# Performance work log

Hardware: AMD Instinct MI355X
Metric: run time of the kernel (lower is better)

Reference implementation:

```python
import jax, jax.numpy as jnp
import numpy as np

N = 100000   # num nodes
E = 1600000  # num edges (before self-loops)
D_IN, D_HID, D_OUT = 128, 128, 64


def _gcn_layer(x, W, b, src, dst, norm):
    # GCNConv: h = x @ W, then normalized sparse aggregation, then bias.
    h = x @ W                              # [N, d_out]
    msg = h[src] * norm[:, None]           # [E+N, d_out] gathered + scaled messages
    out = jax.ops.segment_sum(msg, dst, num_segments=N)  # scatter-add to dst nodes
    return out + b


def reference(x, W1, b1, W2, b2, edge_index):
    src0, dst0 = edge_index[0], edge_index[1]
    # GCNConv adds self-loops by default
    loop = jnp.arange(N, dtype=src0.dtype)
    src = jnp.concatenate([src0, loop])
    dst = jnp.concatenate([dst0, loop])
    # symmetric normalization: deg^{-1/2}[src] * deg^{-1/2}[dst]
    deg = jax.ops.segment_sum(jnp.ones_like(src, dtype=x.dtype), dst, num_segments=N)
    dinv = jnp.where(deg > 0, jax.lax.rsqrt(jnp.maximum(deg, 1.0)), 0.0)
    norm = dinv[src] * dinv[dst]           # [E+N]

    h = jax.nn.relu(_gcn_layer(x, W1, b1, src, dst, norm))
    return _gcn_layer(h, W2, b2, src, dst, norm)


def setup_inputs() -> dict:
    key = jax.random.key(0)
    k1, k2, k3, k4 = jax.random.split(key, 4)
    x = jax.random.normal(k1, (N, D_IN), dtype=jnp.float32)
    # glorot-ish init for weights
    W1 = jax.random.normal(k2, (D_IN, D_HID), dtype=jnp.float32) * (1.0 / np.sqrt(D_IN))
    b1 = jnp.zeros((D_HID,), dtype=jnp.float32)
    W2 = jax.random.normal(k3, (D_HID, D_OUT), dtype=jnp.float32) * (1.0 / np.sqrt(D_HID))
    b2 = jnp.zeros((D_OUT,), dtype=jnp.float32)
    edge_index = jax.random.randint(k4, (2, E), 0, N, dtype=jnp.int64)
    return {"x": x, "W1": W1, "b1": b1, "W2": W2, "b2": b2, "edge_index": edge_index}
```

## Files before the change

### kernel.cpp

```cpp
#include <hip/hip_runtime.h>

static constexpr int NN = 100000;
static constexpr int EE = 1600000;
static constexpr int BSZ = 64;
static constexpr int NB = (NN + BSZ - 1) / BSZ;
static constexpr int BCAP = 2048;
static constexpr int TILE = 2048;
static constexpr int GB = 2048;


__device__ __forceinline__ unsigned short f2bf(float f) {
    unsigned u = __float_as_uint(f);
    u += 0x7FFFu + ((u >> 16) & 1u);
    return (unsigned short)(u >> 16);
}
__device__ __forceinline__ float bfl(unsigned u) { return __uint_as_float(u << 16); }
__device__ __forceinline__ float bfh(unsigned u) { return __uint_as_float(u & 0xFFFF0000u); }

typedef __attribute__((ext_vector_type(8))) short short8;
typedef __attribute__((ext_vector_type(4))) float float4v;
typedef __attribute__((ext_vector_type(4))) float float4n;


__global__ __launch_bounds__(256) void k_init(const float* __restrict__ W1,
                                              const float* __restrict__ W2,
                                              unsigned short* __restrict__ W1t,
                                              unsigned short* __restrict__ W2t,
                                              int* __restrict__ bcur) {
    int idx = blockIdx.x * 256 + threadIdx.x;
    if (idx < 16384) {
        int n = idx >> 7, k = idx & 127;
        W1t[idx] = f2bf(W1[k * 128 + n]);
    } else if (idx < 24576) {
        int j = idx - 16384;
        int n = j >> 7, k = j & 127;
        W2t[j] = f2bf(W2[k * 64 + n]);
    } else if (idx < 24576 + NB) {
        int b = idx - 24576;
        bcur[b] = b * BCAP;
    }
}


__global__ __launch_bounds__(256) void k_bin(const int* __restrict__ src,
                                             const int* __restrict__ dst,
                                             int* __restrict__ bcur,
                                             int* __restrict__ ebuf, int E) {
    constexpr int K = TILE / 256;
    __shared__ int lcnt[NB];
    __shared__ int lbase[NB];
    const int t = threadIdx.x;
    const int e0 = blockIdx.x * TILE;

    for (int i = t; i < NB; i += 256) lcnt[i] = 0;
    __syncthreads();

    int dreg[K], ofs[K];
#pragma unroll
    for (int k = 0; k < K; ++k) {
        int e = e0 + k * 256 + t;
        if (e < E) {
            int d = dst[e];
            dreg[k] = d;
            ofs[k] = atomicAdd(&lcnt[d >> 6], 1);
        } else dreg[k] = -1;
    }
    __syncthreads();

    for (int i = t; i < NB; i += 256) {
        int c = lcnt[i];
        lbase[i] = c ? atomicAdd(&bcur[i], c) : 0;
    }
    __syncthreads();

#pragma unroll
    for (int k = 0; k < K; ++k) {
        if (dreg[k] >= 0) {
            int e = e0 + k * 256 + t;
            int s = src[e];
            int b = dreg[k] >> 6;
            ebuf[lbase[b] + ofs[k]] = (s << 6) | (dreg[k] & 63);
        }
    }
}


__global__ __launch_bounds__(256) void k_csr(const int* __restrict__ bcur,
                                             const int* __restrict__ ebuf,
                                             int2* __restrict__ rbe,
                                             float* __restrict__ dinv,
                                             int* __restrict__ csr, int n) {
    __shared__ int lcnt[BSZ];
    __shared__ int lofs[BSZ];
    const int b = blockIdx.x, t = threadIdx.x;
    if (t < BSZ) lcnt[t] = 0;
    __syncthreads();
    const int beg = b * BCAP, end = bcur[b];
    for (int j = beg + t; j < end; j += 256) atomicAdd(&lcnt[ebuf[j] & 63], 1);
    __syncthreads();
    if (t < BSZ) {
        int c = lcnt[t];
        int x = c;
#pragma unroll
        for (int off = 1; off < 64; off <<= 1) {
            int y = __shfl_up(x, off, 64);
            if (t >= off) x += y;
        }
        int exc = x - c;
        int node = b * BSZ + t;
        if (node < n) {
            rbe[node] = make_int2(beg + exc, beg + exc + c);
            dinv[node] = rsqrtf((float)c + 1.0f);
        }
        lofs[t] = beg + exc;
    }
    __syncthreads();
    for (int j = beg + t; j < end; j += 256) {
        int e = ebuf[j];
        int pos = atomicAdd(&lofs[e & 63], 1);
        csr[pos] = e >> 6;
    }
}


__global__ __launch_bounds__(256) void k_gemm128m(const float* __restrict__ X,
                                                  const unsigned short* __restrict__ W1t,
                                                  const float* __restrict__ dinv,
                                                  unsigned* __restrict__ G, int M) {
    __shared__ float cls[4 * 16 * 132];
    const int t = threadIdx.x;
    const int w = t >> 6, lane = t & 63;
    const int quad = lane >> 4, m16 = lane & 15;
    const int row0 = blockIdx.x * 64 + w * 16;
    int arow = row0 + m16; if (arow >= M) arow = M - 1;

    short8 afrag[4];
#pragma unroll
    for (int ks = 0; ks < 4; ++ks) {
        const float* p = X + (size_t)arow * 128 + ks * 32 + quad * 8;
        float4 u0 = ((const float4*)p)[0];
        float4 u1 = ((const float4*)p)[1];
        short8 a;
        a[0] = (short)f2bf(u0.x); a[1] = (short)f2bf(u0.y);
        a[2] = (short)f2bf(u0.z); a[3] = (short)f2bf(u0.w);
        a[4] = (short)f2bf(u1.x); a[5] = (short)f2bf(u1.y);
        a[6] = (short)f2bf(u1.z); a[7] = (short)f2bf(u1.w);
        afrag[ks] = a;
    }
    float* myc = cls + w * 16 * 132;
#pragma unroll
    for (int nt = 0; nt < 8; ++nt) {
        float4v acc = {0.f, 0.f, 0.f, 0.f};
#pragma unroll
        for (int ks = 0; ks < 4; ++ks) {
            const short8 b = *((const short8*)(W1t + (size_t)(nt * 16 + m16) * 128 + ks * 32 + quad * 8));
            acc = __builtin_amdgcn_mfma_f32_16x16x32_bf16(afrag[ks], b, acc, 0, 0, 0);
        }
#pragma unroll
        for (int r = 0; r < 4; ++r)
            myc[(quad * 4 + r) * 132 + nt * 16 + m16] = acc[r];
    }
    __syncthreads();
#pragma unroll
    for (int i = 0; i < 8; ++i) {
        int idx = i * 64 + lane;
        int r = idx >> 5, c = idx & 31;
        int grow = row0 + r;
        if (grow < M) {
            float4 v = *((const float4*)(myc + r * 132 + c * 4));
            float s = dinv[grow];
            uint2 p;
            p.x = (unsigned)f2bf(v.x * s) | ((unsigned)f2bf(v.y * s) << 16);
            p.y = (unsigned)f2bf(v.z * s) | ((unsigned)f2bf(v.w * s) << 16);
            ((uint2*)G)[(size_t)(c >> 3) * NN * 8 + (size_t)grow * 8 + (c & 7)] = p;
        }
    }
}


__global__ __launch_bounds__(256) void k_gemm64m(const unsigned short* __restrict__ X,
                                                 const unsigned short* __restrict__ W2t,
                                                 const float* __restrict__ dinv,
                                                 unsigned* __restrict__ G, int M) {
    __shared__ float cls[4 * 16 * 68];
    const int t = threadIdx.x;
    const int w = t >> 6, lane = t & 63;
    const int quad = lane >> 4, m16 = lane & 15;
    const int row0 = blockIdx.x * 64 + w * 16;
    int arow = row0 + m16; if (arow >= M) arow = M - 1;

    short8 afrag[4];
#pragma unroll
    for (int ks = 0; ks < 4; ++ks)
        afrag[ks] = *((const short8*)(X + (size_t)ks * NN * 32 + (size_t)arow * 32 + quad * 8));

    float* myc = cls + w * 16 * 68;
#pragma unroll
    for (int nt = 0; nt < 4; ++nt) {
        float4v acc = {0.f, 0.f, 0.f, 0.f};
#pragma unroll
        for (int ks = 0; ks < 4; ++ks) {
            const short8 b = *((const short8*)(W2t + (size_t)(nt * 16 + m16) * 128 + ks * 32 + quad * 8));
            acc = __builtin_amdgcn_mfma_f32_16x16x32_bf16(afrag[ks], b, acc, 0, 0, 0);
        }
#pragma unroll
        for (int r = 0; r < 4; ++r)
            myc[(quad * 4 + r) * 68 + nt * 16 + m16] = acc[r];
    }
    __syncthreads();
#pragma unroll
    for (int i = 0; i < 4; ++i) {
        int idx = i * 64 + lane;
        int r = idx >> 4, c = idx & 15;
        int grow = row0 + r;
        if (grow < M) {
            float4 v = *((const float4*)(myc + r * 68 + c * 4));
            float s = dinv[grow];
            uint2 p;
            p.x = (unsigned)f2bf(v.x * s) | ((unsigned)f2bf(v.y * s) << 16);
            p.y = (unsigned)f2bf(v.z * s) | ((unsigned)f2bf(v.w * s) << 16);
            ((uint2*)G)[(size_t)(c >> 3) * NN * 8 + (size_t)grow * 8 + (c & 7)] = p;
        }
    }
}


__device__ __forceinline__ int2 ld_rbe(const int2* __restrict__ rbe, int node, int n) {
    int2 r = make_int2(0, 0);
    if (node < n) {
        long long v = __builtin_nontemporal_load((const long long*)(rbe + node));
        r.x = (int)(v & 0xffffffffll);
        r.y = (int)(v >> 32);
    }
    return r;
}
__device__ __forceinline__ int ld_csr(const int* __restrict__ csr, int2 re, int off) {
    int deg = re.y - re.x;
    int v = __builtin_nontemporal_load(csr + re.x + ((off < deg) ? off : 0));
    return (deg > 0) ? v : 0;
}

template<int LAYER>
__global__ __launch_bounds__(256) void k_gather_s(
        const int2* __restrict__ rbe, const int* __restrict__ csr,
        const unsigned* __restrict__ Gall, const float* __restrict__ dinv,
        const float* __restrict__ bias, unsigned* __restrict__ OUT, int n) {
    const int lane = threadIdx.x & 63;
    const int w = threadIdx.x >> 6;
    const int l16 = lane & 15;
    const int g2 = (lane >> 3) & 1;
    const int sub = lane & 7;

    int slice, wis, stride;
    if (LAYER == 1) {
        slice = (blockIdx.x & 7) >> 1;
        wis = (blockIdx.x >> 3) * 8 + (blockIdx.x & 1) * 4 + w;
        stride = (GB / 8) * 8;
    } else {
        slice = (blockIdx.x & 7) >> 2;
        wis = (blockIdx.x >> 3) * 16 + (blockIdx.x & 3) * 4 + w;
        stride = (GB / 8) * 16;
    }
    const int iter_nodes = stride * 4;
    const uint2* slab = (const uint2*)(Gall + (size_t)slice * NN * 16);

    int node = wis * 4 + (lane >> 4);
    int2 re_cur = ld_rbe(rbe, node, n);
    int2 re_nx  = ld_rbe(rbe, node + iter_nodes, n);
    int idx_cur = ld_csr(csr, re_cur, l16);

    for (; node < n; node += iter_nodes) {
        const int2 re = re_cur;
        int idx = idx_cur;
        re_cur = re_nx;
        re_nx  = ld_rbe(rbe, node + 2 * iter_nodes, n);
        idx_cur = ld_csr(csr, re_cur, l16);

        const int deg = re.y - re.x;
        int idx2 = (deg > 16) ? ld_csr(csr, re, 16 + l16) : 0;

        float a0 = 0.f, a1 = 0.f, a2 = 0.f, a3 = 0.f;
        int wb = 0;
        bool done = false;
        while (!done) {
#pragma unroll
            for (int half = 0; half < 2 && !done; ++half) {
                const int hbase = wb + half * 16;
                const int hidx = half ? idx2 : idx;
#pragma unroll
                for (int g = 0; g < 2 && !done; ++g) {
#pragma unroll
                    for (int st = 0; st < 4; ++st) {
                        int ew = g * 8 + st * 2 + g2;
                        int e = hbase + ew;
                        int s = __shfl(hidx, (lane & 48) | ew, 64);
                        uint2 v = slab[(size_t)s * 8 + sub];
                        if (e < deg) { a0 += bfl(v.x); a1 += bfh(v.x);
                                       a2 += bfl(v.y); a3 += bfh(v.y); }
                    }
                    if (!__any(hbase + (g + 1) * 8 < deg)) done = true;
                }
            }
            if (!done) {
                wb += 32;
                if (wb >= BCAP) break;
                idx  = ld_csr(csr, re, wb + l16);
                idx2 = (deg > wb + 16) ? ld_csr(csr, re, wb + 16 + l16) : 0;
            }
        }
        a0 += __shfl_xor(a0, 8, 64);
        a1 += __shfl_xor(a1, 8, 64);
        a2 += __shfl_xor(a2, 8, 64);
        a3 += __shfl_xor(a3, 8, 64);
        if (g2 == 0) {
            uint2 vs = slab[(size_t)node * 8 + sub];
            a0 += bfl(vs.x); a1 += bfh(vs.x); a2 += bfl(vs.y); a3 += bfh(vs.y);
            const float di = dinv[node];
            const float4 bv = ((const float4*)bias)[slice * 8 + sub];
            float r0 = fmaf(a0, di, bv.x), r1 = fmaf(a1, di, bv.y);
            float r2 = fmaf(a2, di, bv.z), r3 = fmaf(a3, di, bv.w);
            if (LAYER == 1) {
                r0 = fmaxf(r0, 0.f); r1 = fmaxf(r1, 0.f);
                r2 = fmaxf(r2, 0.f); r3 = fmaxf(r3, 0.f);
                unsigned lo = (unsigned)f2bf(r0) | ((unsigned)f2bf(r1) << 16);
                unsigned hi = (unsigned)f2bf(r2) | ((unsigned)f2bf(r3) << 16);
                unsigned long long p = (unsigned long long)lo | ((unsigned long long)hi << 32);
                __builtin_nontemporal_store(p,
                    (unsigned long long*)((uint2*)OUT + (size_t)slice * NN * 8 + (size_t)node * 8 + sub));
            } else {
                float4n r = {r0, r1, r2, r3};
                __builtin_nontemporal_store(r,
                    (float4n*)OUT + (size_t)node * 16 + slice * 8 + sub);
            }
        }
    }
}


extern "C" void kernel_launch(void* const* d_in, const int* in_sizes, int n_in,
                              void* d_out, int out_size, void* d_ws, size_t ws_size,
                              hipStream_t stream) {
    const float* x  = (const float*)d_in[0];
    const float* W1 = (const float*)d_in[1];
    const float* b1 = (const float*)d_in[2];
    const float* W2 = (const float*)d_in[3];
    const float* b2 = (const float*)d_in[4];
    const int*   ei = (const int*)d_in[5];
    const int* src = ei;
    const int* dst = ei + EE;
    float* out = (float*)d_out;

    unsigned* g1b = (unsigned*)d_ws;
    unsigned* h1b = g1b + (size_t)NN * 64;
    unsigned* g2b = h1b + (size_t)NN * 64;
    unsigned short* w1t = (unsigned short*)(g2b + (size_t)NN * 32);
    unsigned short* w2t = w1t + 16384;
    int2*  rbe  = (int2*)(w2t + 8192);
    float* dinv = (float*)(rbe + NN);
    int*   bcur = (int*)(dinv + NN);
    int*   ebuf = bcur + NB;
    int*   csr  = ebuf + (size_t)NB * BCAP;

    constexpr int IB = (24576 + NB + 255) / 256;

    k_init<<<IB, 256, 0, stream>>>(W1, W2, w1t, w2t, bcur);
    k_bin<<<(EE + TILE - 1) / TILE, 256, 0, stream>>>(src, dst, bcur, ebuf, EE);
    k_csr<<<NB, 256, 0, stream>>>(bcur, ebuf, rbe, dinv, csr, NN);

    k_gemm128m<<<(NN + 63) / 64, 256, 0, stream>>>(x, w1t, dinv, g1b, NN);
    k_gather_s<1><<<GB, 256, 0, stream>>>(rbe, csr, g1b, dinv, b1, h1b, NN);

    k_gemm64m<<<(NN + 63) / 64, 256, 0, stream>>>((const unsigned short*)h1b, w2t, dinv, g2b, NN);
    k_gather_s<2><<<GB, 256, 0, stream>>>(rbe, csr, g2b, dinv, b2, (unsigned*)out, NN);
}
```

Before: 350.7 us.

## Split gather by source-node half to localize feature reads in cache

Each destination's CSR neighbor list is split into two segments by whether the source id is in the low or high half of the node range. The gather then runs as separate passes, one per source half, so each pass touches only half the feature table and its working set fits better in cache. Partial sums from the first pass are stored in fp32 scratch, reusing the g2b and ebuf workspace, and the second pass adds them in and applies scaling, bias and activation. The lane mapping also changes to 8 lanes per node. The price is more kernel launches and extra partial-sum traffic through global memory.

After: 402.3 us. 1.15x slower.

```diff
diff --git a/kernel.cpp b/kernel.cpp
--- a/kernel.cpp
+++ b/kernel.cpp
@@ -1,6 +1,8 @@
 #include <hip/hip_runtime.h>
 
 static constexpr int NN = 100000;
+static constexpr int NH = NN / 2;
+static constexpr int NNH2 = NN / 2;
 static constexpr int EE = 1600000;
 static constexpr int BSZ = 64;
 static constexpr int NB = (NN + BSZ - 1) / BSZ;
@@ -87,19 +89,24 @@
 
 __global__ __launch_bounds__(256) void k_csr(const int* __restrict__ bcur,
                                              const int* __restrict__ ebuf,
-                                             int2* __restrict__ rbe,
+                                             int2* __restrict__ seg0,
+                                             int2* __restrict__ seg1,
                                              float* __restrict__ dinv,
                                              int* __restrict__ csr, int n) {
-    __shared__ int lcnt[BSZ];
-    __shared__ int lofs[BSZ];
+    __shared__ int lcnt_lo[BSZ], lcnt_hi[BSZ];
+    __shared__ int lofs_lo[BSZ], lofs_hi[BSZ];
     const int b = blockIdx.x, t = threadIdx.x;
-    if (t < BSZ) lcnt[t] = 0;
+    if (t < BSZ) { lcnt_lo[t] = 0; lcnt_hi[t] = 0; }
     __syncthreads();
     const int beg = b * BCAP, end = bcur[b];
-    for (int j = beg + t; j < end; j += 256) atomicAdd(&lcnt[ebuf[j] & 63], 1);
+    for (int j = beg + t; j < end; j += 256) {
+        int e = ebuf[j];
+        if ((e >> 6) < NH) atomicAdd(&lcnt_lo[e & 63], 1);
+        else               atomicAdd(&lcnt_hi[e & 63], 1);
+    }
     __syncthreads();
     if (t < BSZ) {
-        int c = lcnt[t];
+        int lo = lcnt_lo[t], hi = lcnt_hi[t], c = lo + hi;
         int x = c;
 #pragma unroll
         for (int off = 1; off < 64; off <<= 1) {
@@ -109,16 +116,19 @@
         int exc = x - c;
         int node = b * BSZ + t;
         if (node < n) {
-            rbe[node] = make_int2(beg + exc, beg + exc + c);
+            seg0[node] = make_int2(beg + exc, beg + exc + lo);
+            seg1[node] = make_int2(beg + exc + lo, beg + exc + c);
             dinv[node] = rsqrtf((float)c + 1.0f);
         }
-        lofs[t] = beg + exc;
+        lofs_lo[t] = beg + exc;
+        lofs_hi[t] = beg + exc + lo;
     }
     __syncthreads();
     for (int j = beg + t; j < end; j += 256) {
         int e = ebuf[j];
-        int pos = atomicAdd(&lofs[e & 63], 1);
-        csr[pos] = e >> 6;
+        int d = e & 63, s = e >> 6;
+        int pos = atomicAdd((s < NH) ? &lofs_lo[d] : &lofs_hi[d], 1);
+        csr[pos] = s;
     }
 }
 
@@ -225,112 +235,131 @@
 }
 
 
-__device__ __forceinline__ int2 ld_rbe(const int2* __restrict__ rbe, int node, int n) {
+__device__ __forceinline__ int2 ld_seg(const int2* __restrict__ seg, int node, int nend) {
     int2 r = make_int2(0, 0);
-    if (node < n) {
-        long long v = __builtin_nontemporal_load((const long long*)(rbe + node));
+    if (node < nend) {
+        long long v = __builtin_nontemporal_load((const long long*)(seg + node));
         r.x = (int)(v & 0xffffffffll);
         r.y = (int)(v >> 32);
     }
     return r;
 }
-__device__ __forceinline__ int ld_csr(const int* __restrict__ csr, int2 re, int off) {
-    int deg = re.y - re.x;
-    int v = __builtin_nontemporal_load(csr + re.x + ((off < deg) ? off : 0));
-    return (deg > 0) ? v : 0;
-}
-
-template<int LAYER>
-__global__ __launch_bounds__(256) void k_gather_s(
-        const int2* __restrict__ rbe, const int* __restrict__ csr,
+__device__ __forceinline__ int ld_csr8(const int* __restrict__ csr, int b, int d, int off) {
+    int o = (off < d) ? off : (d > 0 ? d - 1 : 0);
+    return __builtin_nontemporal_load(csr + b + o);
+}
+
+template<int LAYER, int HALF>
+__global__ __launch_bounds__(256) void k_gather_h(
+        const int2* __restrict__ seg, const int* __restrict__ csr,
         const unsigned* __restrict__ Gall, const float* __restrict__ dinv,
-        const float* __restrict__ bias, unsigned* __restrict__ OUT, int n) {
+        const float* __restrict__ bias, float* __restrict__ Pa,
+        float* __restrict__ Pb, unsigned* __restrict__ OUT,
+        int nbase, int nend) {
     const int lane = threadIdx.x & 63;
     const int w = threadIdx.x >> 6;
-    const int l16 = lane & 15;
-    const int g2 = (lane >> 3) & 1;
-    const int sub = lane & 7;
+    const int l8 = lane & 7;
+    const int shb = lane & 56;
 
     int slice, wis, stride;
     if (LAYER == 1) {
         slice = (blockIdx.x & 7) >> 1;
         wis = (blockIdx.x >> 3) * 8 + (blockIdx.x & 1) * 4 + w;
-        stride = (GB / 8) * 8;
+        stride = 2048;
     } else {
         slice = (blockIdx.x & 7) >> 2;
         wis = (blockIdx.x >> 3) * 16 + (blockIdx.x & 3) * 4 + w;
-        stride = (GB / 8) * 16;
-    }
-    const int iter_nodes = stride * 4;
+        stride = 4096;
+    }
+    const int iter_nodes = stride * 8;
     const uint2* slab = (const uint2*)(Gall + (size_t)slice * NN * 16);
-
-    int node = wis * 4 + (lane >> 4);
-    int2 re_cur = ld_rbe(rbe, node, n);
-    int2 re_nx  = ld_rbe(rbe, node + iter_nodes, n);
-    int idx_cur = ld_csr(csr, re_cur, l16);
-
-    for (; node < n; node += iter_nodes) {
-        const int2 re = re_cur;
+    float* Pbase = (LAYER == 1)
+        ? ((slice < 2 ? Pa : Pb) + (size_t)(slice & 1) * NNH2 * 32)
+        : nullptr;
+
+    int node = nbase + wis * 8 + (lane >> 3);
+    int2 sg_cur = ld_seg(seg, node, nend);
+    int2 sg_nx  = ld_seg(seg, node + iter_nodes, nend);
+    int idx_cur = ld_csr8(csr, sg_cur.x, sg_cur.y - sg_cur.x, l8);
+
+    for (; node < nend; node += iter_nodes) {
+        const int2 sg = sg_cur;
         int idx = idx_cur;
-        re_cur = re_nx;
-        re_nx  = ld_rbe(rbe, node + 2 * iter_nodes, n);
-        idx_cur = ld_csr(csr, re_cur, l16);
-
-        const int deg = re.y - re.x;
-        int idx2 = (deg > 16) ? ld_csr(csr, re, 16 + l16) : 0;
+        sg_cur = sg_nx;
+        sg_nx  = ld_seg(seg, node + 2 * iter_nodes, nend);
+        idx_cur = ld_csr8(csr, sg_cur.x, sg_cur.y - sg_cur.x, l8);
+
+        const int deg = sg.y - sg.x;
+        int idx2 = (deg > 8) ? ld_csr8(csr, sg.x, deg, 8 + l8) : 0;
 
         float a0 = 0.f, a1 = 0.f, a2 = 0.f, a3 = 0.f;
         int wb = 0;
         bool done = false;
         while (!done) {
 #pragma unroll
-            for (int half = 0; half < 2 && !done; ++half) {
-                const int hbase = wb + half * 16;
-                const int hidx = half ? idx2 : idx;
+            for (int hw = 0; hw < 2 && !done; ++hw) {
+                const int hidx = hw ? idx2 : idx;
 #pragma unroll
                 for (int g = 0; g < 2 && !done; ++g) {
 #pragma unroll
                     for (int st = 0; st < 4; ++st) {
-                        int ew = g * 8 + st * 2 + g2;
-                        int e = hbase + ew;
-                        int s = __shfl(hidx, (lane & 48) | ew, 64);
-                        uint2 v = slab[(size_t)s * 8 + sub];
-                        if (e < deg) { a0 += bfl(v.x); a1 += bfh(v.x);
-                                       a2 += bfl(v.y); a3 += bfh(v.y); }
+                        int ew = g * 4 + st;
+                        int e = wb + hw * 8 + ew;
+                        int s = __shfl(hidx, shb | ew, 64);
+                        if (e < deg) {
+                            uint2 v = slab[(size_t)s * 8 + l8];
+                            a0 += bfl(v.x); a1 += bfh(v.x);
+                            a2 += bfl(v.y); a3 += bfh(v.y);
+                        }
                     }
-                    if (!__any(hbase + (g + 1) * 8 < deg)) done = true;
+                    if (!__any(wb + hw * 8 + (g + 1) * 4 < deg)) done = true;
                 }
             }
             if (!done) {
-                wb += 32;
+                wb += 16;
                 if (wb >= BCAP) break;
-                idx  = ld_csr(csr, re, wb + l16);
-                idx2 = (deg > wb + 16) ? ld_csr(csr, re, wb + 16 + l16) : 0;
+                idx  = ld_csr8(csr, sg.x, deg, wb + l8);
+                idx2 = (deg > wb + 8) ? ld_csr8(csr, sg.x, deg, wb + 8 + l8) : 0;
             }
         }
-        a0 += __shfl_xor(a0, 8, 64);
-        a1 += __shfl_xor(a1, 8, 64);
-        a2 += __shfl_xor(a2, 8, 64);
-        a3 += __shfl_xor(a3, 8, 64);
-        if (g2 == 0) {
-            uint2 vs = slab[(size_t)node * 8 + sub];
+        const bool selfhere = (HALF == 0) ? (node < NH) : (node >= NH);
+        if (selfhere) {
+            uint2 vs = slab[(size_t)node * 8 + l8];
             a0 += bfl(vs.x); a1 += bfh(vs.x); a2 += bfl(vs.y); a3 += bfh(vs.y);
-            const float di = dinv[node];
-            const float4 bv = ((const float4*)bias)[slice * 8 + sub];
-            float r0 = fmaf(a0, di, bv.x), r1 = fmaf(a1, di, bv.y);
-            float r2 = fmaf(a2, di, bv.z), r3 = fmaf(a3, di, bv.w);
-            if (LAYER == 1) {
+        }
+        if (LAYER == 1) {
+            float* Pp = Pbase + (size_t)(node - nbase) * 32 + l8 * 4;
+            if (HALF == 0) {
+                float4n r = {a0, a1, a2, a3};
+                __builtin_nontemporal_store(r, (float4n*)Pp);
+            } else {
+                float4n p = __builtin_nontemporal_load((const float4n*)Pp);
+                const float di = __builtin_nontemporal_load(dinv + node);
+                const float4 bv = ((const float4*)bias)[slice * 8 + l8];
+                float r0 = fmaf(a0 + p.x, di, bv.x), r1 = fmaf(a1 + p.y, di, bv.y);
+                float r2 = fmaf(a2 + p.z, di, bv.z), r3 = fmaf(a3 + p.w, di, bv.w);
                 r0 = fmaxf(r0, 0.f); r1 = fmaxf(r1, 0.f);
                 r2 = fmaxf(r2, 0.f); r3 = fmaxf(r3, 0.f);
-                unsigned lo = (unsigned)f2bf(r0) | ((unsigned)f2bf(r1) << 16);
-                unsigned hi = (unsigned)f2bf(r2) | ((unsigned)f2bf(r3) << 16);
-                unsigned long long p = (unsigned long long)lo | ((unsigned long long)hi << 32);
-                __builtin_nontemporal_store(p,
-                    (unsigned long long*)((uint2*)OUT + (size_t)slice * NN * 8 + (size_t)node * 8 + sub));
+                uint2 o;
+                o.x = (unsigned)f2bf(r0) | ((unsigned)f2bf(r1) << 16);
+                o.y = (unsigned)f2bf(r2) | ((unsigned)f2bf(r3) << 16);
+                ((uint2*)OUT)[(size_t)slice * NN * 8 + (size_t)node * 8 + l8] = o;
+            }
+        } else {
+            float* Pp = (float*)OUT + (size_t)node * 64 + slice * 32 + l8 * 4;
+            if (HALF == 0) {
+                float4n r = {a0, a1, a2, a3};
+                __builtin_nontemporal_store(r, (float4n*)Pp);
             } else {
-                float4n r = {r0, r1, r2, r3};
-                __builtin_nontemporal_store(r,
-                    (float4n*)OUT + (size_t)node * 16 + slice * 8 + sub);
+                float4n p = __builtin_nontemporal_load((const float4n*)Pp);
+                const float di = __builtin_nontemporal_load(dinv + node);
+                const float4 bv = ((const float4*)bias)[slice * 8 + l8];
+                float4n r;
+                r.x = fmaf(a0 + p.x, di, bv.x);
+                r.y = fmaf(a1 + p.y, di, bv.y);
+                r.z = fmaf(a2 + p.z, di, bv.z);
+                r.w = fmaf(a3 + p.w, di, bv.w);
+                *(float4n*)Pp = r;
             }
         }
     }
@@ -350,26 +379,34 @@
     const int* dst = ei + EE;
     float* out = (float*)d_out;
 
-    unsigned* g1b = (unsigned*)d_ws;
-    unsigned* h1b = g1b + (size_t)NN * 64;
-    unsigned* g2b = h1b + (size_t)NN * 64;
-    unsigned short* w1t = (unsigned short*)(g2b + (size_t)NN * 32);
-    unsigned short* w2t = w1t + 16384;
-    int2*  rbe  = (int2*)(w2t + 8192);
-    float* dinv = (float*)(rbe + NN);
-    int*   bcur = (int*)(dinv + NN);
-    int*   ebuf = bcur + NB;
-    int*   csr  = ebuf + (size_t)NB * BCAP;
+    char* p = (char*)d_ws;
+    unsigned* g1b = (unsigned*)p;             p += (size_t)NN * 64 * 4;
+    unsigned* h1b = (unsigned*)p;             p += (size_t)NN * 64 * 4;
+    unsigned* g2b = (unsigned*)p;             p += (size_t)NN * 32 * 4;
+    unsigned short* w1t = (unsigned short*)p; p += 16384 * 2;
+    unsigned short* w2t = (unsigned short*)p; p += 8192 * 2;
+    int2*  seg0 = (int2*)p;                   p += (size_t)NN * 8;
+    int2*  seg1 = (int2*)p;                   p += (size_t)NN * 8;
+    float* dinv = (float*)p;                  p += (size_t)NN * 4;
+    int*   bcur = (int*)p;                    p += ((size_t)NB * 4 + 15) & ~(size_t)15;
+    int*   csr  = (int*)p;                    p += (size_t)NB * BCAP * 4;
+    int*   ebuf = (int*)p;
+    float* Pa   = (float*)g2b;
+    float* Pb   = (float*)ebuf;
 
     constexpr int IB = (24576 + NB + 255) / 256;
 
     k_init<<<IB, 256, 0, stream>>>(W1, W2, w1t, w2t, bcur);
     k_bin<<<(EE + TILE - 1) / TILE, 256, 0, stream>>>(src, dst, bcur, ebuf, EE);
-    k_csr<<<NB, 256, 0, stream>>>(bcur, ebuf, rbe, dinv, csr, NN);
+    k_csr<<<NB, 256, 0, stream>>>(bcur, ebuf, seg0, seg1, dinv, csr, NN);
 
     k_gemm128m<<<(NN + 63) / 64, 256, 0, stream>>>(x, w1t, dinv, g1b, NN);
-    k_gather_s<1><<<GB, 256, 0, stream>>>(rbe, csr, g1b, dinv, b1, h1b, NN);
+    k_gather_h<1, 0><<<GB, 256, 0, stream>>>(seg0, csr, g1b, dinv, b1, Pa, Pb, h1b, 0, NNH2);
+    k_gather_h<1, 1><<<GB, 256, 0, stream>>>(seg1, csr, g1b, dinv, b1, Pa, Pb, h1b, 0, NNH2);
+    k_gather_h<1, 0><<<GB, 256, 0, stream>>>(seg0, csr, g1b, dinv, b1, Pa, Pb, h1b, NNH2, NN);
+    k_gather_h<1, 1><<<GB, 256, 0, stream>>>(seg1, csr, g1b, dinv, b1, Pa, Pb, h1b, NNH2, NN);
 
     k_gemm64m<<<(NN + 63) / 64, 256, 0, stream>>>((const unsigned short*)h1b, w2t, dinv, g2b, NN);
-    k_gather_s<2><<<GB, 256, 0, stream>>>(rbe, csr, g2b, dinv, b2, (unsigned*)out, NN);
-}
+    k_gather_h<2, 0><<<GB, 256, 0, stream>>>(seg0, csr, g2b, dinv, b2, Pa, Pb, (unsigned*)out, 0, NN);
+    k_gather_h<2, 1><<<GB, 256, 0, stream>>>(seg1, csr, g2b, dinv, b2, Pa, Pb, (unsigned*)out, 0, NN);
+}
```
